# Kernel optimization log

Measured on AMD Instinct MI355X. Metric: run time of the kernel, lower is better.

Reference implementation:

```python
import jax, jax.numpy as jnp
import numpy as np

N_NODES = 50000
N_EDGES = 800000
F_NODE = 128
F_EDGE = 64
Z_DIM = 2 * F_NODE + F_EDGE  # 320
BN_EPS = 1e-5


def _params(key):
    ks = jax.random.split(key, 16)
    s = 1.0 / np.sqrt(Z_DIM)
    p = {}
    for li, k4 in zip((1, 2), (ks[:8], ks[8:])):
        p[f"Wf{li}"] = jax.random.uniform(k4[0], (Z_DIM, F_NODE), jnp.float32, -s, s)
        p[f"bf{li}"] = jax.random.uniform(k4[1], (F_NODE,), jnp.float32, -s, s)
        p[f"Ws{li}"] = jax.random.uniform(k4[2], (Z_DIM, F_NODE), jnp.float32, -s, s)
        p[f"bs{li}"] = jax.random.uniform(k4[3], (F_NODE,), jnp.float32, -s, s)
        p[f"gamma{li}"] = jnp.ones((F_NODE,), jnp.float32)
        p[f"beta{li}"] = jnp.zeros((F_NODE,), jnp.float32)
        p[f"rmean{li}"] = jax.random.normal(k4[4], (F_NODE,), jnp.float32) * 0.1
        p[f"rvar{li}"] = jax.random.uniform(k4[5], (F_NODE,), jnp.float32, 0.5, 1.5)
    return p


def setup_inputs() -> dict:
    key = jax.random.key(0)
    k1, k2, k3, kp = jax.random.split(key, 4)
    inp = {
        "x": jax.random.normal(k1, (N_NODES, F_NODE), jnp.float32),
        "edge_index": jax.random.randint(k2, (2, N_EDGES), 0, N_NODES, jnp.int64),
        "edge_attr": jax.random.normal(k3, (N_EDGES, F_EDGE), jnp.float32),
    }
    inp.update(_params(kp))
    return inp


def _cgconv(x, src, dst, edge_attr, Wf, bf, Ws, bs, gamma, beta, rmean, rvar):
    # z = [x_i, x_j, edge_attr] with i = target (dst), j = source (src)
    z = jnp.concatenate([x[dst], x[src], edge_attr], axis=-1)  # [E, 320]
    msg = jax.nn.sigmoid(z @ Wf + bf) * jax.nn.softplus(z @ Ws + bs)  # [E, F]
    n = x.shape[0]
    summed = jax.ops.segment_sum(msg, dst, num_segments=n)  # [N, F]
    cnt = jax.ops.segment_sum(jnp.ones((dst.shape[0],), x.dtype), dst, num_segments=n)
    out = summed / jnp.maximum(cnt, 1.0)[:, None]  # mean aggregation
    out = (out - rmean) * jax.lax.rsqrt(rvar + BN_EPS) * gamma + beta  # BN (eval)
    return out + x  # residual


def reference(x, edge_index, edge_attr,
              Wf1, bf1, Ws1, bs1, gamma1, beta1, rmean1, rvar1,
              Wf2, bf2, Ws2, bs2, gamma2, beta2, rmean2, rvar2):
    src, dst = edge_index[0], edge_index[1]
    x = _cgconv(x, src, dst, edge_attr, Wf1, bf1, Ws1, bs1, gamma1, beta1, rmean1, rvar1)
    # dropout_p = 0.0 -> identity
    x = _cgconv(x, src, dst, edge_attr, Wf2, bf2, Ws2, bs2, gamma2, beta2, rmean2, rvar2)
    return x
```

## Files before the change

kernel.cpp:

```cpp
#include <hip/hip_runtime.h>
#include <math.h>

#define FN 128
#define FE 64
#define EPS 1e-5f

typedef __attribute__((ext_vector_type(8))) short bf16x8;
typedef __attribute__((ext_vector_type(4))) float f32x4;

__device__ __forceinline__ float bf2f(unsigned int u_low16) {
    union { unsigned int i; float f; } v; v.i = u_low16 << 16; return v.f;
}
__device__ __forceinline__ float bf2f_hi(unsigned int u) {
    union { unsigned int i; float f; } v; v.i = u & 0xffff0000u; return v.f;
}
__device__ __forceinline__ unsigned short f2bf(float f) {
    union { float f; unsigned int i; } v; v.f = f;
    unsigned int r = v.i + 0x7FFFu + ((v.i >> 16) & 1u);
    return (unsigned short)(r >> 16);
}
__device__ __forceinline__ unsigned int pack2bf(float a, float b) {
    return (unsigned int)f2bf(a) | ((unsigned int)f2bf(b) << 16);
}
__device__ __forceinline__ float actfn(float f, float s) {
    float sig = __builtin_amdgcn_rcpf(1.0f + __expf(-f));
    float sp = fmaxf(s, 0.0f) + __logf(1.0f + __expf(-fabsf(s)));
    return sig * sp;
}

__global__ void hist_kernel(const int* __restrict__ edst, int* __restrict__ hist, int ne) {
    int e = blockIdx.x * 256 + threadIdx.x;
    if (e < ne) atomicAdd(&hist[edst[e]], 1);
}

__global__ __launch_bounds__(1024) void scan_kernel(
    const int* __restrict__ hist, int* __restrict__ cursor, int nn)
{
    __shared__ int buf[1024];
    int t = threadIdx.x;
    int per = (nn + 1023) >> 10;
    int lo = t * per, hi = min(lo + per, nn);
    int s = 0;
    for (int i = lo; i < hi; i++) s += hist[i];
    buf[t] = s;
    __syncthreads();
    int incl = s;
    for (int off = 1; off < 1024; off <<= 1) {
        int tmp = (t >= off) ? buf[t - off] : 0;
        __syncthreads();
        incl += tmp;
        buf[t] = incl;
        __syncthreads();
    }
    int run = incl - s;
    for (int i = lo; i < hi; i++) { cursor[i] = run; run += hist[i]; }
}

__global__ void scatter_kernel(const int* __restrict__ edst, int* __restrict__ cursor,
                               int* __restrict__ perm, int ne)
{
    int e = blockIdx.x * 256 + threadIdx.x;
    if (e < ne) {
        int pos = atomicAdd(&cursor[edst[e]], 1);
        perm[pos] = e;
    }
}

__global__ __launch_bounds__(256) void node_gemm(
    const float* __restrict__ X, const float* __restrict__ Wf,
    const float* __restrict__ Ws, unsigned short* __restrict__ A, int nnodes)
{
    __shared__ float Xs[16][129];
    __shared__ float Bs[16][68];
    const int t = threadIdx.x;
    const int m0 = blockIdx.x * 128;
    const int c0 = blockIdx.y * 64;
    const int part = c0 >> 7;
    const int cp0 = c0 & 127;
    const float* Bsrc = ((part < 2) ? Wf : Ws) + (part & 1) * 128 * 128 + cp0;
    const int tm = t >> 4, tn = t & 15;
    float acc[8][4];
#pragma unroll
    for (int i = 0; i < 8; i++)
#pragma unroll
        for (int j = 0; j < 4; j++) acc[i][j] = 0.0f;

    for (int k0 = 0; k0 < 128; k0 += 16) {
        {
            int ml = t & 127;
            int kq0 = (t >> 7) * 2;
#pragma unroll
            for (int q = 0; q < 2; q++) {
                int kq = kq0 + q;
                float4 v = make_float4(0.f, 0.f, 0.f, 0.f);
                int m = m0 + ml;
                if (m < nnodes) v = *(const float4*)(X + (size_t)m * FN + k0 + kq * 4);
                Xs[kq * 4 + 0][ml] = v.x; Xs[kq * 4 + 1][ml] = v.y;
                Xs[kq * 4 + 2][ml] = v.z; Xs[kq * 4 + 3][ml] = v.w;
            }
            int kk = t >> 4, j4 = (t & 15) * 4;
            float4 b = *(const float4*)(Bsrc + (size_t)(k0 + kk) * FN + j4);
            Bs[kk][j4 + 0] = b.x; Bs[kk][j4 + 1] = b.y;
            Bs[kk][j4 + 2] = b.z; Bs[kk][j4 + 3] = b.w;
        }
        __syncthreads();
#pragma unroll
        for (int kk = 0; kk < 16; kk++) {
            float xv[8], bv[4];
#pragma unroll
            for (int i = 0; i < 8; i++) xv[i] = Xs[kk][tm * 8 + i];
#pragma unroll
            for (int j = 0; j < 4; j++) bv[j] = Bs[kk][tn * 4 + j];
#pragma unroll
            for (int i = 0; i < 8; i++)
#pragma unroll
                for (int j = 0; j < 4; j++) acc[i][j] = fmaf(xv[i], bv[j], acc[i][j]);
        }
        __syncthreads();
    }
#pragma unroll
    for (int i = 0; i < 8; i++) {
        int m = m0 + tm * 8 + i;
        if (m < nnodes) {
            size_t base = (size_t)m * 512 + c0 + tn * 4;
#pragma unroll
            for (int j = 0; j < 4; j++) A[base + j] = f2bf(acc[i][j]);
        }
    }
}

__global__ __launch_bounds__(256, 2) void edge_kernel(
    const unsigned short* __restrict__ A, const float* __restrict__ EA,
    const int* __restrict__ esrc, const int* __restrict__ edst,
    const int* __restrict__ perm,
    const float* __restrict__ Wf, const float* __restrict__ Ws,
    const float* __restrict__ bfv, const float* __restrict__ bsv,
    float* __restrict__ summed, int nedges)
{
    __shared__ unsigned short Wlds[2][128][64];
    __shared__ unsigned short Ebuf[4][64][36];

    const int t = threadIdx.x;
    const int w = t >> 6, lane = t & 63;
    const int ebase = blockIdx.x * 256 + w * 64;

    {
        int col = t & 127;
        int half = t >> 7;
        int swz = (col & 7) << 3;
#pragma unroll 2
        for (int mat = 0; mat < 2; mat++) {
            const float* Wsrc = (mat == 0 ? Wf : Ws) + 256 * FN + col;
#pragma unroll
            for (int q = 0; q < 16; q++) {
                int k = half * 32 + q * 2;
                unsigned int u = pack2bf(Wsrc[(size_t)k * FN], Wsrc[(size_t)(k + 1) * FN]);
                *(unsigned int*)&Wlds[mat][col][k ^ swz] = u;
            }
        }
    }

    int e = ebase + lane;
    bool valid = (e < nedges);
    int eC = valid ? e : (nedges - 1);
    const int pe = perm[eC];
    const int mydst = edst[pe];
    const int mysrc = esrc[pe];

    int vmask[4];
    const unsigned short* dB[4];
    const unsigned short* sB[4];
#pragma unroll
    for (int nt = 0; nt < 4; nt++) {
        int el = nt * 16 + (lane & 15);
        vmask[nt] = (ebase + el < nedges) ? 1 : 0;
        int dn = __shfl(mydst, el);
        int sn = __shfl(mysrc, el);
        dB[nt] = A + (size_t)dn * 512;
        sB[nt] = A + (size_t)sn * 512 + 128;
    }

    bf16x8 Eb[4][2];
    {
        const int koff = (lane >> 4) << 3;
#pragma unroll
        for (int nt = 0; nt < 4; nt++) {
            int el = nt * 16 + (lane & 15);
            int pr = __shfl(pe, el);
            const float* p = EA + (size_t)pr * FE + koff;
#pragma unroll
            for (int kk = 0; kk < 2; kk++) {
                float4 v0 = *(const float4*)(p + kk * 32);
                float4 v1 = *(const float4*)(p + kk * 32 + 4);
                bf16x8 b;
                b[0] = (short)f2bf(v0.x); b[1] = (short)f2bf(v0.y);
                b[2] = (short)f2bf(v0.z); b[3] = (short)f2bf(v0.w);
                b[4] = (short)f2bf(v1.x); b[5] = (short)f2bf(v1.y);
                b[6] = (short)f2bf(v1.z); b[7] = (short)f2bf(v1.w);
                Eb[nt][kk] = b;
            }
        }
    }
    __syncthreads();

    const int colo = (lane >> 4) << 2;

#pragma unroll 1
    for (int cb = 0; cb < 4; cb++) {
        const int c0 = cb * 32;

        uint2 gdf[4][2], gsf[4][2], gds[4][2], gss[4][2];
#pragma unroll
        for (int nt = 0; nt < 4; nt++)
#pragma unroll
            for (int mt = 0; mt < 2; mt++) {
                int off = c0 + mt * 16 + colo;
                gdf[nt][mt] = *(const uint2*)(const void*)(dB[nt] + off);
                gsf[nt][mt] = *(const uint2*)(const void*)(sB[nt] + off);
                gds[nt][mt] = *(const uint2*)(const void*)(dB[nt] + 256 + off);
                gss[nt][mt] = *(const uint2*)(const void*)(sB[nt] + 256 + off);
            }

        float4 bF[2], bS[2];
#pragma unroll
        for (int mt = 0; mt < 2; mt++) {
            bF[mt] = *(const float4*)(bfv + c0 + mt * 16 + colo);
            bS[mt] = *(const float4*)(bsv + c0 + mt * 16 + colo);
        }

        f32x4 accF[2][4], accS[2][4];
#pragma unroll
        for (int mt = 0; mt < 2; mt++)
#pragma unroll
            for (int nt = 0; nt < 4; nt++) {
                accF[mt][nt] = (f32x4){bF[mt].x, bF[mt].y, bF[mt].z, bF[mt].w};
                accS[mt][nt] = (f32x4){bS[mt].x, bS[mt].y, bS[mt].z, bS[mt].w};
            }
#pragma unroll
        for (int kk = 0; kk < 2; kk++) {
            bf16x8 aF[2], aS[2];
#pragma unroll
            for (int mt = 0; mt < 2; mt++) {
                int col = c0 + mt * 16 + (lane & 15);
                int kidx = ((kk << 5) + ((lane >> 4) << 3)) ^ ((col & 7) << 3);
                aF[mt] = *(const bf16x8*)&Wlds[0][col][kidx];
                aS[mt] = *(const bf16x8*)&Wlds[1][col][kidx];
            }
#pragma unroll
            for (int mt = 0; mt < 2; mt++)
#pragma unroll
                for (int nt = 0; nt < 4; nt++) {
                    accF[mt][nt] = __builtin_amdgcn_mfma_f32_16x16x32_bf16(
                        aF[mt], Eb[nt][kk], accF[mt][nt], 0, 0, 0);
                    accS[mt][nt] = __builtin_amdgcn_mfma_f32_16x16x32_bf16(
                        aS[mt], Eb[nt][kk], accS[mt][nt], 0, 0, 0);
                }
        }

#pragma unroll
        for (int nt = 0; nt < 4; nt++) {
            int edge = nt * 16 + (lane & 15);
#pragma unroll
            for (int mt = 0; mt < 2; mt++) {
                f32x4 F = accF[mt][nt], S = accS[mt][nt];
                uint2 a0 = gdf[nt][mt], a1 = gsf[nt][mt];
                uint2 b0 = gds[nt][mt], b1 = gss[nt][mt];
                F[0] += bf2f(a0.x & 0xffffu) + bf2f(a1.x & 0xffffu);
                F[1] += bf2f_hi(a0.x)        + bf2f_hi(a1.x);
                F[2] += bf2f(a0.y & 0xffffu) + bf2f(a1.y & 0xffffu);
                F[3] += bf2f_hi(a0.y)        + bf2f_hi(a1.y);
                S[0] += bf2f(b0.x & 0xffffu) + bf2f(b1.x & 0xffffu);
                S[1] += bf2f_hi(b0.x)        + bf2f_hi(b1.x);
                S[2] += bf2f(b0.y & 0xffffu) + bf2f(b1.y & 0xffffu);
                S[3] += bf2f_hi(b0.y)        + bf2f_hi(b1.y);
                float m0 = actfn(F[0], S[0]);
                float m1 = actfn(F[1], S[1]);
                float m2 = actfn(F[2], S[2]);
                float m3 = actfn(F[3], S[3]);
                if (!vmask[nt]) { m0 = m1 = m2 = m3 = 0.0f; }
                uint2 mw = make_uint2(pack2bf(m0, m1), pack2bf(m2, m3));
                *(uint2*)&Ebuf[w][edge][mt * 16 + colo] = mw;
            }
        }

        {
            int h = lane >> 5, cc = lane & 31;
            int base_e = h << 5;
            float run = 0.f;
            int prev = __shfl(mydst, base_e);
#pragma unroll 1
            for (int q = 0; q < 32; q++) {
                int e2 = base_e + q;
                int d2 = __shfl(mydst, e2);
                float v = bf2f((unsigned int)Ebuf[w][e2][cc]);
                if (d2 != prev) {
                    atomicAdd(&summed[(size_t)prev * FN + c0 + cc], run);
                    run = 0.f; prev = d2;
                }
                run += v;
            }
            atomicAdd(&summed[(size_t)prev * FN + c0 + cc], run);
        }
    }
}

__global__ __launch_bounds__(256) void finalize_kernel(
    const float* __restrict__ summed, const int* __restrict__ hist,
    const float* xin,
    const float* __restrict__ gamma, const float* __restrict__ beta,
    const float* __restrict__ rmean, const float* __restrict__ rvar,
    float* out, int nnodes)
{
    int idx = blockIdx.x * 256 + threadIdx.x;
    if (idx >= nnodes * FN) return;
    int n = idx >> 7, c = idx & (FN - 1);
    float cnt = (float)hist[n];
    float mean = summed[idx] / fmaxf(cnt, 1.0f);
    float y = (mean - rmean[c]) * rsqrtf(rvar[c] + EPS) * gamma[c] + beta[c] + xin[idx];
    out[idx] = y;
}

extern "C" void kernel_launch(void* const* d_in, const int* in_sizes, int n_in,
                              void* d_out, int out_size, void* d_ws, size_t ws_size,
                              hipStream_t stream)
{
    const float* x    = (const float*)d_in[0];
    const int*   eidx = (const int*)d_in[1];
    const float* ea   = (const float*)d_in[2];
    const float* Wf1 = (const float*)d_in[3],  * bf1 = (const float*)d_in[4];
    const float* Ws1 = (const float*)d_in[5],  * bs1 = (const float*)d_in[6];
    const float* g1  = (const float*)d_in[7],  * be1 = (const float*)d_in[8];
    const float* rm1 = (const float*)d_in[9],  * rv1 = (const float*)d_in[10];
    const float* Wf2 = (const float*)d_in[11], * bf2 = (const float*)d_in[12];
    const float* Ws2 = (const float*)d_in[13], * bs2 = (const float*)d_in[14];
    const float* g2  = (const float*)d_in[15], * be2 = (const float*)d_in[16];
    const float* rm2 = (const float*)d_in[17], * rv2 = (const float*)d_in[18];
    float* out = (float*)d_out;

    const int NN = in_sizes[0] / FN;
    const int NE = in_sizes[2] / FE;
    const int* esrc = eidx;
    const int* edst = eidx + NE;

    char* wsp = (char*)d_ws;
    unsigned short* A = (unsigned short*)wsp;            wsp += (size_t)NN * 512 * 2;
    float* summed     = (float*)wsp;                     wsp += (size_t)NN * FN * 4;
    int* hist         = (int*)wsp;                       wsp += (size_t)NN * 4;
    int* perm         = (int*)wsp;                       wsp += (size_t)NE * 4;
    int* cursor       = (int*)summed;

    const int egrid = (NE + 255) / 256;
    const int ngrid = (NN + 127) / 128;
    const int fgrid = (NN * FN + 255) / 256;

    (void)hipMemsetAsync(hist, 0, (size_t)NN * 4, stream);
    hist_kernel<<<egrid, 256, 0, stream>>>(edst, hist, NE);
    scan_kernel<<<1, 1024, 0, stream>>>(hist, cursor, NN);
    scatter_kernel<<<egrid, 256, 0, stream>>>(edst, cursor, perm, NE);

    (void)hipMemsetAsync(summed, 0, (size_t)NN * FN * 4, stream);
    node_gemm<<<dim3(ngrid, 8), 256, 0, stream>>>(x, Wf1, Ws1, A, NN);
    edge_kernel<<<egrid, 256, 0, stream>>>(A, ea, esrc, edst, perm, Wf1, Ws1, bf1, bs1, summed, NE);
    finalize_kernel<<<fgrid, 256, 0, stream>>>(summed, hist, x, g1, be1, rm1, rv1, out, NN);

    (void)hipMemsetAsync(summed, 0, (size_t)NN * FN * 4, stream);
    node_gemm<<<dim3(ngrid, 8), 256, 0, stream>>>(out, Wf2, Ws2, A, NN);
    edge_kernel<<<egrid, 256, 0, stream>>>(A, ea, esrc, edst, perm, Wf2, Ws2, bf2, bs2, summed, NE);
    finalize_kernel<<<fgrid, 256, 0, stream>>>(summed, hist, out, g2, be2, rm2, rv2, out, NN);
}
```

Measured before the change: 872.9 us.

## Use MFMA for node GEMM and shrink edge-kernel scatter buffer

Rewrites the node projection GEMM to convert X and W tiles to bf16 in swizzled LDS and compute with 16x16x32 bf16 MFMA instead of scalar FP32 FMAs. In the edge kernel, the per-wave message buffer shrinks to one 16-edge tile, and segmented reduction runs per tile using a precomputed ballot mask of destination changes. This lowers LDS use so occupancy can rise to four blocks per CU. The trade-off is more atomics at 8-edge boundaries and reliance on wave-level LDS ordering, fenced only by compiler barriers, with no explicit sync.

```diff
diff --git a/kernel.cpp b/kernel.cpp
--- a/kernel.cpp
+++ b/kernel.cpp
@@ -66,70 +66,93 @@
     }
 }
 
-__global__ __launch_bounds__(256) void node_gemm(
+__global__ __launch_bounds__(256, 4) void node_gemm(
     const float* __restrict__ X, const float* __restrict__ Wf,
     const float* __restrict__ Ws, unsigned short* __restrict__ A, int nnodes)
 {
-    __shared__ float Xs[16][129];
-    __shared__ float Bs[16][68];
+    __shared__ unsigned short Xs[128][128];
+    __shared__ unsigned short Wt[64][128];
     const int t = threadIdx.x;
     const int m0 = blockIdx.x * 128;
     const int c0 = blockIdx.y * 64;
     const int part = c0 >> 7;
-    const int cp0 = c0 & 127;
-    const float* Bsrc = ((part < 2) ? Wf : Ws) + (part & 1) * 128 * 128 + cp0;
-    const int tm = t >> 4, tn = t & 15;
-    float acc[8][4];
-#pragma unroll
-    for (int i = 0; i < 8; i++)
-#pragma unroll
-        for (int j = 0; j < 4; j++) acc[i][j] = 0.0f;
-
-    for (int k0 = 0; k0 < 128; k0 += 16) {
-        {
-            int ml = t & 127;
-            int kq0 = (t >> 7) * 2;
-#pragma unroll
-            for (int q = 0; q < 2; q++) {
-                int kq = kq0 + q;
-                float4 v = make_float4(0.f, 0.f, 0.f, 0.f);
-                int m = m0 + ml;
-                if (m < nnodes) v = *(const float4*)(X + (size_t)m * FN + k0 + kq * 4);
-                Xs[kq * 4 + 0][ml] = v.x; Xs[kq * 4 + 1][ml] = v.y;
-                Xs[kq * 4 + 2][ml] = v.z; Xs[kq * 4 + 3][ml] = v.w;
-            }
-            int kk = t >> 4, j4 = (t & 15) * 4;
-            float4 b = *(const float4*)(Bsrc + (size_t)(k0 + kk) * FN + j4);
-            Bs[kk][j4 + 0] = b.x; Bs[kk][j4 + 1] = b.y;
-            Bs[kk][j4 + 2] = b.z; Bs[kk][j4 + 3] = b.w;
-        }
-        __syncthreads();
-#pragma unroll
-        for (int kk = 0; kk < 16; kk++) {
-            float xv[8], bv[4];
-#pragma unroll
-            for (int i = 0; i < 8; i++) xv[i] = Xs[kk][tm * 8 + i];
-#pragma unroll
-            for (int j = 0; j < 4; j++) bv[j] = Bs[kk][tn * 4 + j];
-#pragma unroll
-            for (int i = 0; i < 8; i++)
-#pragma unroll
-                for (int j = 0; j < 4; j++) acc[i][j] = fmaf(xv[i], bv[j], acc[i][j]);
-        }
-        __syncthreads();
-    }
-#pragma unroll
-    for (int i = 0; i < 8; i++) {
-        int m = m0 + tm * 8 + i;
-        if (m < nnodes) {
-            size_t base = (size_t)m * 512 + c0 + tn * 4;
-#pragma unroll
-            for (int j = 0; j < 4; j++) A[base + j] = f2bf(acc[i][j]);
-        }
-    }
-}
-
-__global__ __launch_bounds__(256, 2) void edge_kernel(
+    const float* Bsrc = ((part < 2) ? Wf : Ws) + (part & 1) * 128 * 128 + (c0 & 127);
+
+    {
+        int row = t & 127;
+        int kh = t >> 7;
+        int m = m0 + row;
+        const float* src = X + (size_t)(m < nnodes ? m : 0) * FN + kh * 64;
+        int swz = (row & 7) << 3;
+#pragma unroll
+        for (int q = 0; q < 8; q++) {
+            float4 v0 = *(const float4*)(src + q * 8);
+            float4 v1 = *(const float4*)(src + q * 8 + 4);
+            unsigned int u0 = pack2bf(v0.x, v0.y), u1 = pack2bf(v0.z, v0.w);
+            unsigned int u2 = pack2bf(v1.x, v1.y), u3 = pack2bf(v1.z, v1.w);
+            int kk = (kh * 64 + q * 8) ^ swz;
+            *(uint4*)&Xs[row][kk] = make_uint4(u0, u1, u2, u3);
+        }
+    }
+    {
+        int n = t & 63;
+        int kq = t >> 6;
+        int swz = (n & 7) << 3;
+#pragma unroll
+        for (int q = 0; q < 16; q++) {
+            int k = kq * 32 + q * 2;
+            unsigned int u = pack2bf(Bsrc[(size_t)k * FN + n], Bsrc[(size_t)(k + 1) * FN + n]);
+            *(unsigned int*)&Wt[n][k ^ swz] = u;
+        }
+    }
+    __syncthreads();
+
+    const int wv = t >> 6, lane = t & 63;
+    const int mw = (wv & 1) * 64;
+    const int nw = (wv >> 1) * 32;
+    f32x4 acc[4][2];
+#pragma unroll
+    for (int mt = 0; mt < 4; mt++)
+#pragma unroll
+        for (int nt = 0; nt < 2; nt++) acc[mt][nt] = (f32x4){0.f, 0.f, 0.f, 0.f};
+
+#pragma unroll
+    for (int ks = 0; ks < 4; ks++) {
+        int kb = ks * 32 + ((lane >> 4) << 3);
+        bf16x8 a[4], b[2];
+#pragma unroll
+        for (int mt = 0; mt < 4; mt++) {
+            int row = mw + mt * 16 + (lane & 15);
+            a[mt] = *(const bf16x8*)&Xs[row][kb ^ ((row & 7) << 3)];
+        }
+#pragma unroll
+        for (int nt = 0; nt < 2; nt++) {
+            int n = nw + nt * 16 + (lane & 15);
+            b[nt] = *(const bf16x8*)&Wt[n][kb ^ ((n & 7) << 3)];
+        }
+#pragma unroll
+        for (int mt = 0; mt < 4; mt++)
+#pragma unroll
+            for (int nt = 0; nt < 2; nt++)
+                acc[mt][nt] = __builtin_amdgcn_mfma_f32_16x16x32_bf16(
+                    a[mt], b[nt], acc[mt][nt], 0, 0, 0);
+    }
+
+#pragma unroll
+    for (int mt = 0; mt < 4; mt++) {
+        int m = m0 + mw + mt * 16 + ((lane >> 4) << 2);
+#pragma unroll
+        for (int nt = 0; nt < 2; nt++) {
+            int n = c0 + nw + nt * 16 + (lane & 15);
+#pragma unroll
+            for (int r = 0; r < 4; r++)
+                if (m + r < nnodes)
+                    A[(size_t)(m + r) * 512 + n] = f2bf(acc[mt][nt][r]);
+        }
+    }
+}
+
+__global__ __launch_bounds__(256, 4) void edge_kernel(
     const unsigned short* __restrict__ A, const float* __restrict__ EA,
     const int* __restrict__ esrc, const int* __restrict__ edst,
     const int* __restrict__ perm,
@@ -138,7 +161,7 @@
     float* __restrict__ summed, int nedges)
 {
     __shared__ unsigned short Wlds[2][128][64];
-    __shared__ unsigned short Ebuf[4][64][36];
+    __shared__ unsigned short Ebuf[4][16][36];
 
     const int t = threadIdx.x;
     const int w = t >> 6, lane = t & 63;
@@ -166,6 +189,13 @@
     const int pe = perm[eC];
     const int mydst = edst[pe];
     const int mysrc = esrc[pe];
+
+    unsigned long long flushAfter;
+    {
+        int prevd = __shfl(mydst, (lane + 63) & 63);
+        unsigned long long chg = __ballot(lane > 0 && (mydst != prevd));
+        flushAfter = (chg >> 1) | (1ull << 63);
+    }
 
     int vmask[4];
     const unsigned short* dB[4];
@@ -204,6 +234,8 @@
     __syncthreads();
 
     const int colo = (lane >> 4) << 2;
+    const int cc = lane & 31;
+    const int h = lane >> 5;
 
 #pragma unroll 1
     for (int cb = 0; cb < 4; cb++) {
@@ -259,7 +291,7 @@
 
 #pragma unroll
         for (int nt = 0; nt < 4; nt++) {
-            int edge = nt * 16 + (lane & 15);
+            int eg = lane & 15;
 #pragma unroll
             for (int mt = 0; mt < 2; mt++) {
                 f32x4 F = accF[mt][nt], S = accS[mt][nt];
@@ -279,27 +311,27 @@
                 float m3 = actfn(F[3], S[3]);
                 if (!vmask[nt]) { m0 = m1 = m2 = m3 = 0.0f; }
                 uint2 mw = make_uint2(pack2bf(m0, m1), pack2bf(m2, m3));
-                *(uint2*)&Ebuf[w][edge][mt * 16 + colo] = mw;
-            }
-        }
-
-        {
-            int h = lane >> 5, cc = lane & 31;
-            int base_e = h << 5;
-            float run = 0.f;
-            int prev = __shfl(mydst, base_e);
-#pragma unroll 1
-            for (int q = 0; q < 32; q++) {
-                int e2 = base_e + q;
-                int d2 = __shfl(mydst, e2);
-                float v = bf2f((unsigned int)Ebuf[w][e2][cc]);
-                if (d2 != prev) {
-                    atomicAdd(&summed[(size_t)prev * FN + c0 + cc], run);
-                    run = 0.f; prev = d2;
+                *(uint2*)&Ebuf[w][eg][mt * 16 + colo] = mw;
+            }
+
+            asm volatile("" ::: "memory");
+
+            {
+                int ebit0 = nt * 16 + h * 8;
+                float run = 0.f;
+#pragma unroll
+                for (int q = 0; q < 8; q++) {
+                    run += bf2f((unsigned int)Ebuf[w][h * 8 + q][cc]);
+                    int d = __shfl(mydst, ebit0 + q);
+                    bool fl = (q == 7) || ((flushAfter >> (ebit0 + q)) & 1ull);
+                    if (fl) {
+                        atomicAdd(&summed[(size_t)d * FN + c0 + cc], run);
+                        run = 0.f;
+                    }
                 }
-                run += v;
-            }
-            atomicAdd(&summed[(size_t)prev * FN + c0 + cc], run);
+            }
+
+            asm volatile("" ::: "memory");
         }
     }
 }
```

New measurement: 1.232 ms. +41.2%, slower.
